# Performance work log

Hardware: AMD Instinct MI355X
Metric: run time of the kernel (lower is better)

## Reference

```python
import jax, jax.numpy as jnp
import numpy as np

V = 100000   # vocab size
H = 1280     # GRU hidden / pic_emb_size
E = 300      # word_emb_size
L = 32       # max_length


def setup_inputs() -> dict:
    key = jax.random.key(0)
    ks = jax.random.split(key, 7)
    s = 0.02  # weight init scale
    return {
        "hidden0": jax.random.normal(ks[0], (H,), jnp.float32),
        "start_emb": jax.random.normal(ks[1], (E,), jnp.float32),
        "W_ih": jax.random.normal(ks[2], (3 * H, E), jnp.float32) * s,
        "W_hh": jax.random.normal(ks[3], (3 * H, H), jnp.float32) * s,
        "b_ih": jnp.zeros((3 * H,), jnp.float32),
        "b_hh": jnp.zeros((3 * H,), jnp.float32),
        "W_cls": jax.random.normal(ks[4], (V, H), jnp.float32) * s,
        "b_cls": jnp.zeros((V,), jnp.float32),
        "vocab_vectors": jax.random.normal(ks[5], (V, E), jnp.float32),
        "max_length": L,
    }


def reference(hidden0, start_emb, W_ih, W_hh, b_ih, b_hh, W_cls, b_cls,
              vocab_vectors, max_length):
    """Autoregressive GRU decode: GRU step -> 1280x100k classifier GEMV ->
    argmax -> embedding gather, for max_length steps (batch=1).
    EOS (token 0) emulated with a `done` mask instead of a Python break.
    Returns (tokens [L] int32, hiddens [L, H] float32)."""

    def step(carry, _):
        h, emb, done = carry
        # PyTorch GRU gate layout: [reset | update | new]
        gi = W_ih @ emb + b_ih               # [3H]
        gh = W_hh @ h + b_hh                 # [3H]
        r = jax.nn.sigmoid(gi[:H] + gh[:H])
        z = jax.nn.sigmoid(gi[H:2 * H] + gh[H:2 * H])
        n = jnp.tanh(gi[2 * H:] + r * gh[2 * H:])
        h_new = jnp.where(done, h, (1.0 - z) * n + z * h)
        logits = W_cls @ h_new + b_cls       # [V] classifier GEMV
        pred = jnp.argmax(logits).astype(jnp.int32)
        token = jnp.where(done, 0, pred)
        done_new = done | (pred == 0)
        emb_new = jnp.where(done_new, emb, vocab_vectors[pred])  # gather next word emb
        return (h_new, emb_new, done_new), (token, h_new)

    init = (hidden0, start_emb, jnp.array(False))
    _, (tokens, hiddens) = jax.lax.scan(step, init, None, length=max_length)
    return tokens, hiddens
```

## Files before the change

kernel.cpp:

```cpp
#include <hip/hip_runtime.h>
#include <math.h>
#include <limits.h>

#define V 100000
#define H 1280
#define E 300
#define L 32
#define G3 (3*H)
#define NBLK 6250

#define WS_H      0
#define WS_EMB    1280
#define WS_GI     1600
#define WS_GH     (WS_GI + G3)
#define WS_SUMABS 9280
#define WS_DONE   9281
#define WS_LOGITS 9284
#define WS_SROW   (WS_LOGITS + V)
#define WS_PLO    (WS_SROW + V)
#define WS_PHI    (WS_PLO + NBLK)
#define WS_Q_BYTEOFF ((size_t)(WS_PHI + NBLK) * 4)
#define WS_BYTES_NEEDED (WS_Q_BYTEOFF + (size_t)V * H)
#define CAND_CAP  256

#define NPART     6250
#define WS_PVAL   WS_LOGITS
#define WS_PIDX   (WS_LOGITS + NPART)

__global__ __launch_bounds__(256)
void init_state(const float* __restrict__ hidden0, const float* __restrict__ start_emb,
                float* __restrict__ ws) {
    int i = blockIdx.x * blockDim.x + threadIdx.x;
    if (i < H) ws[WS_H + i] = hidden0[i];
    if (i < E) ws[WS_EMB + i] = start_emb[i];
    if (i == 0) ((int*)ws)[WS_DONE] = 0;
}

__global__ __launch_bounds__(256)
void convert_int8(const float* __restrict__ W, uint* __restrict__ q_out,
                  float* __restrict__ ws) {
    const int wave = threadIdx.x >> 6;
    const int lane = threadIdx.x & 63;
    const int row = blockIdx.x * 4 + wave;
    const float4* __restrict__ wr = (const float4*)(W + (size_t)row * H);

    float4 v[5];
    float mx = 0.f;
    #pragma unroll
    for (int k = 0; k < 5; ++k) {
        v[k] = wr[lane + 64*k];
        mx = fmaxf(mx, fmaxf(fmaxf(fabsf(v[k].x), fabsf(v[k].y)),
                             fmaxf(fabsf(v[k].z), fabsf(v[k].w))));
    }
    #pragma unroll
    for (int off = 32; off; off >>= 1) mx = fmaxf(mx, __shfl_xor(mx, off));

    float inv = (mx > 0.f) ? 127.0f / mx : 0.f;
    float s   = (mx > 0.f) ? mx / 127.0f : 0.f;

    uint* __restrict__ qrow = q_out + (size_t)row * (H/4);
    #pragma unroll
    for (int k = 0; k < 5; ++k) {
        int q0 = max(-127, min(127, __float2int_rn(v[k].x * inv)));
        int q1 = max(-127, min(127, __float2int_rn(v[k].y * inv)));
        int q2 = max(-127, min(127, __float2int_rn(v[k].z * inv)));
        int q3 = max(-127, min(127, __float2int_rn(v[k].w * inv)));
        qrow[lane + 64*k] = (uint)(q0 & 0xff) | ((uint)(q1 & 0xff) << 8) |
                            ((uint)(q2 & 0xff) << 16) | ((uint)(q3 & 0xff) << 24);
    }
    if (lane == 0) ws[WS_SROW + row] = s;
}

__global__ __launch_bounds__(256)
void gru_matvec(const float* __restrict__ W_ih, const float* __restrict__ W_hh,
                const float* __restrict__ b_ih, const float* __restrict__ b_hh,
                float* __restrict__ ws) {
    if (blockIdx.x == 0 && threadIdx.x == 0) ws[WS_SUMABS] = 0.f;

    const int wave = threadIdx.x >> 6;
    const int lane = threadIdx.x & 63;
    const int row = blockIdx.x * 4 + wave;

    const float4* __restrict__ emb4 = (const float4*)(ws + WS_EMB);
    const float4* __restrict__ h4   = (const float4*)(ws + WS_H);

    const float4* __restrict__ wi = (const float4*)(W_ih + (size_t)row * E);
    float s1 = 0.f;
    for (int i = lane; i < 75; i += 64) {
        float4 w = wi[i], e = emb4[i];
        s1 += w.x*e.x + w.y*e.y + w.z*e.z + w.w*e.w;
    }
    const float4* __restrict__ wh = (const float4*)(W_hh + (size_t)row * H);
    float s2 = 0.f;
    #pragma unroll
    for (int k = 0; k < 5; ++k) {
        float4 w = wh[lane + 64*k], hv = h4[lane + 64*k];
        s2 += w.x*hv.x + w.y*hv.y + w.z*hv.z + w.w*hv.w;
    }
    #pragma unroll
    for (int off = 32; off; off >>= 1) {
        s1 += __shfl_down(s1, off);
        s2 += __shfl_down(s2, off);
    }
    if (lane == 0) {
        ws[WS_GI + row] = s1 + b_ih[row];
        ws[WS_GH + row] = s2 + b_hh[row];
    }
}

__global__ __launch_bounds__(256)
void gru_combine(float* __restrict__ ws, float* __restrict__ hid_out) {
    __shared__ float red[256];
    int tid = threadIdx.x;
    int j = blockIdx.x * 256 + tid;
    int done = ((const int*)ws)[WS_DONE];
    float gir = ws[WS_GI + j], giz = ws[WS_GI + H + j], gin = ws[WS_GI + 2*H + j];
    float ghr = ws[WS_GH + j], ghz = ws[WS_GH + H + j], ghn = ws[WS_GH + 2*H + j];
    float r = 1.f / (1.f + expf(-(gir + ghr)));
    float z = 1.f / (1.f + expf(-(giz + ghz)));
    float n = tanhf(gin + r * ghn);
    float hold = ws[WS_H + j];
    float hnew = done ? hold : (1.f - z) * n + z * hold;
    ws[WS_H + j] = hnew;
    hid_out[j] = hnew;
    red[tid] = fabsf(hnew);
    __syncthreads();
    for (int s = 128; s; s >>= 1) {
        if (tid < s) red[tid] += red[tid + s];
        __syncthreads();
    }
    if (tid == 0) atomicAdd(ws + WS_SUMABS, red[0]);
}

__global__ __launch_bounds__(256)
void cls_int8(const uint* __restrict__ Q, const float* __restrict__ b_cls,
              float* __restrict__ ws) {
    const int wave = threadIdx.x >> 6;
    const int lane = threadIdx.x & 63;
    const int row0 = blockIdx.x * 16 + wave * 4;
    const float4* __restrict__ h4 = (const float4*)(ws + WS_H);

    float4 hv[5];
    #pragma unroll
    for (int k = 0; k < 5; ++k) hv[k] = h4[lane + 64*k];

    const float sumabs = ws[WS_SUMABS];
    float wlo = -INFINITY, whi = -INFINITY;

    for (int rr = 0; rr < 4; ++rr) {
        const int row = row0 + rr;
        const uint* __restrict__ qr = Q + (size_t)row * (H/4);
        float acc = 0.f;
        #pragma unroll
        for (int k = 0; k < 5; ++k) {
            uint u = qr[lane + 64*k];
            float f0 = (float)((int)(u << 24) >> 24);
            float f1 = (float)((int)(u << 16) >> 24);
            float f2 = (float)((int)(u <<  8) >> 24);
            float f3 = (float)((int) u        >> 24);
            acc += f0*hv[k].x + f1*hv[k].y + f2*hv[k].z + f3*hv[k].w;
        }
        #pragma unroll
        for (int off = 32; off; off >>= 1) acc += __shfl_down(acc, off);
        if (lane == 0) {
            float s = ws[WS_SROW + row];
            float q = s * acc + b_cls[row];
            ws[WS_LOGITS + row] = q;
            float e = 0.501f * s * sumabs + 0.002f;
            wlo = fmaxf(wlo, q - e);
            whi = fmaxf(whi, q + e);
        }
    }
    __shared__ float slo[4], shi[4];
    if (lane == 0) { slo[wave] = wlo; shi[wave] = whi; }
    __syncthreads();
    if (threadIdx.x == 0) {
        ws[WS_PLO + blockIdx.x] = fmaxf(fmaxf(slo[0], slo[1]), fmaxf(slo[2], slo[3]));
        ws[WS_PHI + blockIdx.x] = fmaxf(fmaxf(shi[0], shi[1]), fmaxf(shi[2], shi[3]));
    }
}

__global__ __launch_bounds__(1024)
void screen_finalize(float* __restrict__ ws, const float* __restrict__ W_cls,
                     const float* __restrict__ b_cls, const float* __restrict__ vocab,
                     float* __restrict__ tok_out, int t) {
    __shared__ float red[1024];
    __shared__ int   cnt;
    __shared__ int   cidx[CAND_CAP];
    __shared__ float cval[CAND_CAP];
    __shared__ int   s_pred, s_done_new;
    const int tid = threadIdx.x;

    float m = -INFINITY;
    for (int b = tid; b < NBLK; b += 1024) m = fmaxf(m, ws[WS_PLO + b]);
    red[tid] = m;
    __syncthreads();
    for (int s = 512; s; s >>= 1) {
        if (tid < s) red[tid] = fmaxf(red[tid], red[tid + s]);
        __syncthreads();
    }
    m = red[0];
    if (tid == 0) cnt = 0;
    __syncthreads();

    const float sumabs = ws[WS_SUMABS];
    for (int b = tid; b < NBLK; b += 1024) {
        if (ws[WS_PHI + b] >= m) {
            for (int r = b * 16; r < b * 16 + 16; ++r) {
                float s = ws[WS_SROW + r];
                float e = 0.501f * s * sumabs + 0.002f;
                if (ws[WS_LOGITS + r] + e >= m) {
                    int p = atomicAdd(&cnt, 1);
                    if (p < CAND_CAP) cidx[p] = r;
                }
            }
        }
    }
    __syncthreads();
    const int nc = min(cnt, CAND_CAP);

    const int wave = tid >> 6;
    const int lane = tid & 63;
    const float4* __restrict__ h4 = (const float4*)(ws + WS_H);
    for (int c = wave; c < nc; c += 16) {
        int row = cidx[c];
        const float4* __restrict__ wr = (const float4*)(W_cls + (size_t)row * H);
        float s = 0.f;
        #pragma unroll
        for (int k = 0; k < 5; ++k) {
            float4 wv = wr[lane + 64*k], hvv = h4[lane + 64*k];
            s += wv.x*hvv.x + wv.y*hvv.y + wv.z*hvv.z + wv.w*hvv.w;
        }
        #pragma unroll
        for (int off = 32; off; off >>= 1) s += __shfl_down(s, off);
        if (lane == 0) cval[c] = s + b_cls[row];
    }
    __syncthreads();

    if (tid == 0) {
        float bv = -INFINITY; int bi = INT_MAX;
        for (int c = 0; c < nc; ++c) {
            float v = cval[c]; int i = cidx[c];
            if (v > bv || (v == bv && i < bi)) { bv = v; bi = i; }
        }
        int done = ((const int*)ws)[WS_DONE];
        int pred = bi;
        tok_out[t] = (float)(done ? 0 : pred);
        int dn = done | (pred == 0);
        ((int*)ws)[WS_DONE] = dn;
        s_pred = pred; s_done_new = dn;
    }
    __syncthreads();
    if (!s_done_new && tid < E)
        ws[WS_EMB + tid] = vocab[(size_t)s_pred * E + tid];
}

__global__ __launch_bounds__(256)
void logits_argmax_partial(const float* __restrict__ W_cls,
                           const float* __restrict__ b_cls,
                           float* __restrict__ ws) {
    const int wave = threadIdx.x >> 6;
    const int lane = threadIdx.x & 63;
    const int row0 = blockIdx.x * 16 + wave * 4;
    const float4* __restrict__ h4 = (const float4*)(ws + WS_H);

    float best = -INFINITY;
    int bidx = INT_MAX;
    for (int rr = 0; rr < 4; ++rr) {
        const int row = row0 + rr;
        const float4* __restrict__ wr = (const float4*)(W_cls + (size_t)row * H);
        float s = 0.f;
        #pragma unroll
        for (int k = 0; k < 5; ++k) {
            float4 w = wr[lane + 64*k], hv = h4[lane + 64*k];
            s += w.x*hv.x + w.y*hv.y + w.z*hv.z + w.w*hv.w;
        }
        #pragma unroll
        for (int off = 32; off; off >>= 1) s += __shfl_down(s, off);
        if (lane == 0) {
            float logit = s + b_cls[row];
            if (logit > best) { best = logit; bidx = row; }
        }
    }
    __shared__ float sval[4];
    __shared__ int   sidx[4];
    if (lane == 0) { sval[wave] = best; sidx[wave] = bidx; }
    __syncthreads();
    if (threadIdx.x == 0) {
        float bv = sval[0]; int bi = sidx[0];
        #pragma unroll
        for (int w = 1; w < 4; ++w) {
            if (sval[w] > bv || (sval[w] == bv && sidx[w] < bi)) { bv = sval[w]; bi = sidx[w]; }
        }
        ws[WS_PVAL + blockIdx.x] = bv;
        ((int*)ws)[WS_PIDX + blockIdx.x] = bi;
    }
}

__global__ __launch_bounds__(1024)
void argmax_update(float* __restrict__ ws, const float* __restrict__ vocab,
                   float* __restrict__ tok_out, int t) {
    __shared__ float sval[1024];
    __shared__ int   sidx[1024];
    const int tid = threadIdx.x;
    float best = -INFINITY;
    int bidx = INT_MAX;
    for (int i = tid; i < NPART; i += 1024) {
        float v = ws[WS_PVAL + i];
        int  id = ((const int*)ws)[WS_PIDX + i];
        if (v > best || (v == best && id < bidx)) { best = v; bidx = id; }
    }
    sval[tid] = best; sidx[tid] = bidx;
    __syncthreads();
    #pragma unroll
    for (int s = 512; s; s >>= 1) {
        if (tid < s) {
            if (sval[tid+s] > sval[tid] ||
                (sval[tid+s] == sval[tid] && sidx[tid+s] < sidx[tid])) {
                sval[tid] = sval[tid+s]; sidx[tid] = sidx[tid+s];
            }
        }
        __syncthreads();
    }
    __shared__ int s_pred, s_donenew;
    if (tid == 0) {
        int pred = sidx[0];
        int done = ((const int*)ws)[WS_DONE];
        tok_out[t] = (float)(done ? 0 : pred);
        int done_new = done | (pred == 0);
        ((int*)ws)[WS_DONE] = done_new;
        s_pred = pred; s_donenew = done_new;
    }
    __syncthreads();
    if (!s_donenew && tid < E) {
        ws[WS_EMB + tid] = vocab[(size_t)s_pred * E + tid];
    }
}

extern "C" void kernel_launch(void* const* d_in, const int* in_sizes, int n_in,
                              void* d_out, int out_size, void* d_ws, size_t ws_size,
                              hipStream_t stream) {
    const float* hidden0   = (const float*)d_in[0];
    const float* start_emb = (const float*)d_in[1];
    const float* W_ih      = (const float*)d_in[2];
    const float* W_hh      = (const float*)d_in[3];
    const float* b_ih      = (const float*)d_in[4];
    const float* b_hh      = (const float*)d_in[5];
    const float* W_cls     = (const float*)d_in[6];
    const float* b_cls     = (const float*)d_in[7];
    const float* vocab     = (const float*)d_in[8];
    float* out = (float*)d_out;
    float* ws  = (float*)d_ws;

    hipLaunchKernelGGL(init_state, dim3(5), dim3(256), 0, stream, hidden0, start_emb, ws);

    if (ws_size >= WS_BYTES_NEEDED) {
        uint* Q = (uint*)((char*)d_ws + WS_Q_BYTEOFF);
        hipLaunchKernelGGL(convert_int8, dim3(V/4), dim3(256), 0, stream, W_cls, Q, ws);
        for (int t = 0; t < L; ++t) {
            hipLaunchKernelGGL(gru_matvec, dim3(G3/4), dim3(256), 0, stream,
                               W_ih, W_hh, b_ih, b_hh, ws);
            hipLaunchKernelGGL(gru_combine, dim3(5), dim3(256), 0, stream,
                               ws, out + L + (size_t)t * H);
            hipLaunchKernelGGL(cls_int8, dim3(NBLK), dim3(256), 0, stream,
                               Q, b_cls, ws);
            hipLaunchKernelGGL(screen_finalize, dim3(1), dim3(1024), 0, stream,
                               ws, W_cls, b_cls, vocab, out, t);
        }
    } else {
        for (int t = 0; t < L; ++t) {
            hipLaunchKernelGGL(gru_matvec, dim3(G3/4), dim3(256), 0, stream,
                               W_ih, W_hh, b_ih, b_hh, ws);
            hipLaunchKernelGGL(gru_combine, dim3(5), dim3(256), 0, stream,
                               ws, out + L + (size_t)t * H);
            hipLaunchKernelGGL(logits_argmax_partial, dim3(NPART), dim3(256), 0, stream,
                               W_cls, b_cls, ws);
            hipLaunchKernelGGL(argmax_update, dim3(1), dim3(1024), 0, stream,
                               ws, vocab, out, t);
        }
    }
}
```

Measured before the change: 1.860 ms.

## Fuse GRU matvec and gate combine, enlarge classifier blocks, double-buffer hidden

Merges the GRU matvec and gate-combine kernels into one kernel, with one block per hidden unit computing the three gate rows and applying the nonlinearity. This removes a launch and the global round-trip for the gate vectors on each step. The hidden state is ping-ponged between two buffers so the fused kernel can read the old state while writing the new one. The |h| sum is spread over 8 padded atomic slots, and the int8 classifier now does 64 rows per block, which changes the screening granularity used by finalize. Finalize first gathers the passing blocks and then scans their rows in parallel.

```diff
diff --git a/kernel.cpp b/kernel.cpp
--- a/kernel.cpp
+++ b/kernel.cpp
@@ -6,33 +6,35 @@
 #define H 1280
 #define E 300
 #define L 32
-#define G3 (3*H)
-#define NBLK 6250
-
-#define WS_H      0
-#define WS_EMB    1280
-#define WS_GI     1600
-#define WS_GH     (WS_GI + G3)
-#define WS_SUMABS 9280
-#define WS_DONE   9281
-#define WS_LOGITS 9284
+#define NBLK 1563
+
+#define WS_H0     0
+#define WS_H1     1280
+#define WS_EMB    2560
+#define WS_SUM8   2880
+#define WS_DONE   3008
+#define WS_LOGITS 3012
 #define WS_SROW   (WS_LOGITS + V)
 #define WS_PLO    (WS_SROW + V)
 #define WS_PHI    (WS_PLO + NBLK)
-#define WS_Q_BYTEOFF ((size_t)(WS_PHI + NBLK) * 4)
+#define WS_Q_BYTEOFF 824576
 #define WS_BYTES_NEEDED (WS_Q_BYTEOFF + (size_t)V * H)
 #define CAND_CAP  256
-
-#define NPART     6250
-#define WS_PVAL   WS_LOGITS
-#define WS_PIDX   (WS_LOGITS + NPART)
+#define PBLK_CAP  128
+
+#define FB_GI     4000
+#define FB_GH     (FB_GI + 3840)
+#define FB_NPART  6250
+#define FB_PVAL   12000
+#define FB_PIDX   (FB_PVAL + FB_NPART)
 
 __global__ __launch_bounds__(256)
 void init_state(const float* __restrict__ hidden0, const float* __restrict__ start_emb,
                 float* __restrict__ ws) {
     int i = blockIdx.x * blockDim.x + threadIdx.x;
-    if (i < H) ws[WS_H + i] = hidden0[i];
+    if (i < H) ws[WS_H0 + i] = hidden0[i];
     if (i < E) ws[WS_EMB + i] = start_emb[i];
+    if (i < 8) ws[WS_SUM8 + i * 16] = 0.f;
     if (i == 0) ((int*)ws)[WS_DONE] = 0;
 }
 
@@ -71,84 +73,77 @@
     if (lane == 0) ws[WS_SROW + row] = s;
 }
 
-__global__ __launch_bounds__(256)
-void gru_matvec(const float* __restrict__ W_ih, const float* __restrict__ W_hh,
-                const float* __restrict__ b_ih, const float* __restrict__ b_hh,
-                float* __restrict__ ws) {
-    if (blockIdx.x == 0 && threadIdx.x == 0) ws[WS_SUMABS] = 0.f;
-
+__global__ __launch_bounds__(192)
+void gru_fused(const float* __restrict__ W_ih, const float* __restrict__ W_hh,
+               const float* __restrict__ b_ih, const float* __restrict__ b_hh,
+               float* __restrict__ ws, const float* __restrict__ hin,
+               float* __restrict__ hout, float* __restrict__ hid_out) {
+    const int g = threadIdx.x >> 6;
+    const int lane = threadIdx.x & 63;
+    const int j = blockIdx.x;
+    const int row = g * H + j;
+
+    const float4* __restrict__ emb4 = (const float4*)(ws + WS_EMB);
+    const float4* __restrict__ h4   = (const float4*)hin;
+
+    const float4* __restrict__ wi = (const float4*)(W_ih + (size_t)row * E);
+    float si = 0.f;
+    for (int i = lane; i < 75; i += 64) {
+        float4 w = wi[i], e = emb4[i];
+        si += w.x*e.x + w.y*e.y + w.z*e.z + w.w*e.w;
+    }
+    const float4* __restrict__ wh = (const float4*)(W_hh + (size_t)row * H);
+    float sh = 0.f;
+    #pragma unroll
+    for (int k = 0; k < 5; ++k) {
+        float4 w = wh[lane + 64*k], hv = h4[lane + 64*k];
+        sh += w.x*hv.x + w.y*hv.y + w.z*hv.z + w.w*hv.w;
+    }
+    #pragma unroll
+    for (int off = 32; off; off >>= 1) {
+        si += __shfl_down(si, off);
+        sh += __shfl_down(sh, off);
+    }
+    __shared__ float gi_s[3], gh_s[3];
+    if (lane == 0) {
+        gi_s[g] = si + b_ih[row];
+        gh_s[g] = sh + b_hh[row];
+    }
+    __syncthreads();
+    if (threadIdx.x == 0) {
+        float r = 1.f / (1.f + expf(-(gi_s[0] + gh_s[0])));
+        float z = 1.f / (1.f + expf(-(gi_s[1] + gh_s[1])));
+        float n = tanhf(gi_s[2] + r * gh_s[2]);
+        int done = ((const int*)ws)[WS_DONE];
+        float hold = hin[j];
+        float hnew = done ? hold : (1.f - z) * n + z * hold;
+        hout[j] = hnew;
+        hid_out[j] = hnew;
+        atomicAdd(ws + WS_SUM8 + (j & 7) * 16, fabsf(hnew));
+    }
+}
+
+__global__ __launch_bounds__(256)
+void cls_int8(const uint* __restrict__ Q, const float* __restrict__ b_cls,
+              float* __restrict__ ws, const float* __restrict__ h) {
     const int wave = threadIdx.x >> 6;
     const int lane = threadIdx.x & 63;
-    const int row = blockIdx.x * 4 + wave;
-
-    const float4* __restrict__ emb4 = (const float4*)(ws + WS_EMB);
-    const float4* __restrict__ h4   = (const float4*)(ws + WS_H);
-
-    const float4* __restrict__ wi = (const float4*)(W_ih + (size_t)row * E);
-    float s1 = 0.f;
-    for (int i = lane; i < 75; i += 64) {
-        float4 w = wi[i], e = emb4[i];
-        s1 += w.x*e.x + w.y*e.y + w.z*e.z + w.w*e.w;
-    }
-    const float4* __restrict__ wh = (const float4*)(W_hh + (size_t)row * H);
-    float s2 = 0.f;
-    #pragma unroll
-    for (int k = 0; k < 5; ++k) {
-        float4 w = wh[lane + 64*k], hv = h4[lane + 64*k];
-        s2 += w.x*hv.x + w.y*hv.y + w.z*hv.z + w.w*hv.w;
-    }
-    #pragma unroll
-    for (int off = 32; off; off >>= 1) {
-        s1 += __shfl_down(s1, off);
-        s2 += __shfl_down(s2, off);
-    }
-    if (lane == 0) {
-        ws[WS_GI + row] = s1 + b_ih[row];
-        ws[WS_GH + row] = s2 + b_hh[row];
-    }
-}
-
-__global__ __launch_bounds__(256)
-void gru_combine(float* __restrict__ ws, float* __restrict__ hid_out) {
-    __shared__ float red[256];
-    int tid = threadIdx.x;
-    int j = blockIdx.x * 256 + tid;
-    int done = ((const int*)ws)[WS_DONE];
-    float gir = ws[WS_GI + j], giz = ws[WS_GI + H + j], gin = ws[WS_GI + 2*H + j];
-    float ghr = ws[WS_GH + j], ghz = ws[WS_GH + H + j], ghn = ws[WS_GH + 2*H + j];
-    float r = 1.f / (1.f + expf(-(gir + ghr)));
-    float z = 1.f / (1.f + expf(-(giz + ghz)));
-    float n = tanhf(gin + r * ghn);
-    float hold = ws[WS_H + j];
-    float hnew = done ? hold : (1.f - z) * n + z * hold;
-    ws[WS_H + j] = hnew;
-    hid_out[j] = hnew;
-    red[tid] = fabsf(hnew);
-    __syncthreads();
-    for (int s = 128; s; s >>= 1) {
-        if (tid < s) red[tid] += red[tid + s];
-        __syncthreads();
-    }
-    if (tid == 0) atomicAdd(ws + WS_SUMABS, red[0]);
-}
-
-__global__ __launch_bounds__(256)
-void cls_int8(const uint* __restrict__ Q, const float* __restrict__ b_cls,
-              float* __restrict__ ws) {
-    const int wave = threadIdx.x >> 6;
-    const int lane = threadIdx.x & 63;
-    const int row0 = blockIdx.x * 16 + wave * 4;
-    const float4* __restrict__ h4 = (const float4*)(ws + WS_H);
+    const int row0 = blockIdx.x * 64 + wave * 16;
+    const float4* __restrict__ h4 = (const float4*)h;
 
     float4 hv[5];
     #pragma unroll
     for (int k = 0; k < 5; ++k) hv[k] = h4[lane + 64*k];
 
-    const float sumabs = ws[WS_SUMABS];
+    float sumabs = 0.f;
+    #pragma unroll
+    for (int i = 0; i < 8; ++i) sumabs += ws[WS_SUM8 + i * 16];
+
     float wlo = -INFINITY, whi = -INFINITY;
 
-    for (int rr = 0; rr < 4; ++rr) {
+    for (int rr = 0; rr < 16; ++rr) {
         const int row = row0 + rr;
+        if (row >= V) break;
         const uint* __restrict__ qr = Q + (size_t)row * (H/4);
         float acc = 0.f;
         #pragma unroll
@@ -181,16 +176,21 @@
 }
 
 __global__ __launch_bounds__(1024)
-void screen_finalize(float* __restrict__ ws, const float* __restrict__ W_cls,
-                     const float* __restrict__ b_cls, const float* __restrict__ vocab,
-                     float* __restrict__ tok_out, int t) {
+void finalize(float* __restrict__ ws, const float* __restrict__ W_cls,
+              const float* __restrict__ b_cls, const float* __restrict__ vocab,
+              float* __restrict__ tok_out, int t, const float* __restrict__ h) {
     __shared__ float red[1024];
-    __shared__ int   cnt;
+    __shared__ int   npass, cnt;
+    __shared__ int   pblk[PBLK_CAP];
     __shared__ int   cidx[CAND_CAP];
     __shared__ float cval[CAND_CAP];
     __shared__ int   s_pred, s_done_new;
     const int tid = threadIdx.x;
 
+    float sumabs = 0.f;
+    #pragma unroll
+    for (int i = 0; i < 8; ++i) sumabs += ws[WS_SUM8 + i * 16];
+
     float m = -INFINITY;
     for (int b = tid; b < NBLK; b += 1024) m = fmaxf(m, ws[WS_PLO + b]);
     red[tid] = m;
@@ -200,19 +200,26 @@
         __syncthreads();
     }
     m = red[0];
-    if (tid == 0) cnt = 0;
-    __syncthreads();
-
-    const float sumabs = ws[WS_SUMABS];
+    if (tid == 0) { npass = 0; cnt = 0; }
+    __syncthreads();
+
     for (int b = tid; b < NBLK; b += 1024) {
         if (ws[WS_PHI + b] >= m) {
-            for (int r = b * 16; r < b * 16 + 16; ++r) {
-                float s = ws[WS_SROW + r];
-                float e = 0.501f * s * sumabs + 0.002f;
-                if (ws[WS_LOGITS + r] + e >= m) {
-                    int p = atomicAdd(&cnt, 1);
-                    if (p < CAND_CAP) cidx[p] = r;
-                }
+            int p = atomicAdd(&npass, 1);
+            if (p < PBLK_CAP) pblk[p] = b;
+        }
+    }
+    __syncthreads();
+    const int np = min(npass, PBLK_CAP);
+
+    for (int k = tid; k < np * 64; k += 1024) {
+        int row = pblk[k >> 6] * 64 + (k & 63);
+        if (row < V) {
+            float s = ws[WS_SROW + row];
+            float e = 0.501f * s * sumabs + 0.002f;
+            if (ws[WS_LOGITS + row] + e >= m) {
+                int p = atomicAdd(&cnt, 1);
+                if (p < CAND_CAP) cidx[p] = row;
             }
         }
     }
@@ -221,7 +228,7 @@
 
     const int wave = tid >> 6;
     const int lane = tid & 63;
-    const float4* __restrict__ h4 = (const float4*)(ws + WS_H);
+    const float4* __restrict__ h4 = (const float4*)h;
     for (int c = wave; c < nc; c += 16) {
         int row = cidx[c];
         const float4* __restrict__ wr = (const float4*)(W_cls + (size_t)row * H);
@@ -253,17 +260,65 @@
     __syncthreads();
     if (!s_done_new && tid < E)
         ws[WS_EMB + tid] = vocab[(size_t)s_pred * E + tid];
-}
-
-__global__ __launch_bounds__(256)
-void logits_argmax_partial(const float* __restrict__ W_cls,
-                           const float* __restrict__ b_cls,
-                           float* __restrict__ ws) {
+    if (tid < 8) ws[WS_SUM8 + tid * 16] = 0.f;
+}
+
+__global__ __launch_bounds__(256)
+void fb_gru_matvec(const float* __restrict__ W_ih, const float* __restrict__ W_hh,
+                   const float* __restrict__ b_ih, const float* __restrict__ b_hh,
+                   float* __restrict__ ws) {
+    const int wave = threadIdx.x >> 6;
+    const int lane = threadIdx.x & 63;
+    const int row = blockIdx.x * 4 + wave;
+    const float4* __restrict__ emb4 = (const float4*)(ws + WS_EMB);
+    const float4* __restrict__ h4   = (const float4*)(ws + WS_H0);
+    const float4* __restrict__ wi = (const float4*)(W_ih + (size_t)row * E);
+    float s1 = 0.f;
+    for (int i = lane; i < 75; i += 64) {
+        float4 w = wi[i], e = emb4[i];
+        s1 += w.x*e.x + w.y*e.y + w.z*e.z + w.w*e.w;
+    }
+    const float4* __restrict__ wh = (const float4*)(W_hh + (size_t)row * H);
+    float s2 = 0.f;
+    #pragma unroll
+    for (int k = 0; k < 5; ++k) {
+        float4 w = wh[lane + 64*k], hv = h4[lane + 64*k];
+        s2 += w.x*hv.x + w.y*hv.y + w.z*hv.z + w.w*hv.w;
+    }
+    #pragma unroll
+    for (int off = 32; off; off >>= 1) {
+        s1 += __shfl_down(s1, off);
+        s2 += __shfl_down(s2, off);
+    }
+    if (lane == 0) {
+        ws[FB_GI + row] = s1 + b_ih[row];
+        ws[FB_GH + row] = s2 + b_hh[row];
+    }
+}
+
+__global__ __launch_bounds__(256)
+void fb_gru_combine(float* __restrict__ ws, float* __restrict__ hid_out) {
+    int j = blockIdx.x * 256 + threadIdx.x;
+    if (j >= H) return;
+    int done = ((const int*)ws)[WS_DONE];
+    float gir = ws[FB_GI + j], giz = ws[FB_GI + H + j], gin = ws[FB_GI + 2*H + j];
+    float ghr = ws[FB_GH + j], ghz = ws[FB_GH + H + j], ghn = ws[FB_GH + 2*H + j];
+    float r = 1.f / (1.f + expf(-(gir + ghr)));
+    float z = 1.f / (1.f + expf(-(giz + ghz)));
+    float n = tanhf(gin + r * ghn);
+    float hold = ws[WS_H0 + j];
+    float hnew = done ? hold : (1.f - z) * n + z * hold;
+    ws[WS_H0 + j] = hnew;
+    hid_out[j] = hnew;
+}
+
+__global__ __launch_bounds__(256)
+void fb_logits_argmax(const float* __restrict__ W_cls, const float* __restrict__ b_cls,
+                      float* __restrict__ ws) {
     const int wave = threadIdx.x >> 6;
     const int lane = threadIdx.x & 63;
     const int row0 = blockIdx.x * 16 + wave * 4;
-    const float4* __restrict__ h4 = (const float4*)(ws + WS_H);
-
+    const float4* __restrict__ h4 = (const float4*)(ws + WS_H0);
     float best = -INFINITY;
     int bidx = INT_MAX;
     for (int rr = 0; rr < 4; ++rr) {
@@ -289,25 +344,24 @@
     if (threadIdx.x == 0) {
         float bv = sval[0]; int bi = sidx[0];
         #pragma unroll
-        for (int w = 1; w < 4; ++w) {
+        for (int w = 1; w < 4; ++w)
             if (sval[w] > bv || (sval[w] == bv && sidx[w] < bi)) { bv = sval[w]; bi = sidx[w]; }
-        }
-        ws[WS_PVAL + blockIdx.x] = bv;
-        ((int*)ws)[WS_PIDX + blockIdx.x] = bi;
+        ws[FB_PVAL + blockIdx.x] = bv;
+        ((int*)ws)[FB_PIDX + blockIdx.x] = bi;
     }
 }
 
 __global__ __launch_bounds__(1024)
-void argmax_update(float* __restrict__ ws, const float* __restrict__ vocab,
-                   float* __restrict__ tok_out, int t) {
+void fb_argmax_update(float* __restrict__ ws, const float* __restrict__ vocab,
+                      float* __restrict__ tok_out, int t) {
     __shared__ float sval[1024];
     __shared__ int   sidx[1024];
     const int tid = threadIdx.x;
     float best = -INFINITY;
     int bidx = INT_MAX;
-    for (int i = tid; i < NPART; i += 1024) {
-        float v = ws[WS_PVAL + i];
-        int  id = ((const int*)ws)[WS_PIDX + i];
+    for (int i = tid; i < FB_NPART; i += 1024) {
+        float v = ws[FB_PVAL + i];
+        int  id = ((const int*)ws)[FB_PIDX + i];
         if (v > best || (v == best && id < bidx)) { best = v; bidx = id; }
     }
     sval[tid] = best; sidx[tid] = bidx;
@@ -332,9 +386,8 @@
         s_pred = pred; s_donenew = done_new;
     }
     __syncthreads();
-    if (!s_donenew && tid < E) {
+    if (!s_donenew && tid < E)
         ws[WS_EMB + tid] = vocab[(size_t)s_pred * E + tid];
-    }
 }
 
 extern "C" void kernel_launch(void* const* d_in, const int* in_sizes, int n_in,
@@ -358,24 +411,25 @@
         uint* Q = (uint*)((char*)d_ws + WS_Q_BYTEOFF);
         hipLaunchKernelGGL(convert_int8, dim3(V/4), dim3(256), 0, stream, W_cls, Q, ws);
         for (int t = 0; t < L; ++t) {
-            hipLaunchKernelGGL(gru_matvec, dim3(G3/4), dim3(256), 0, stream,
-                               W_ih, W_hh, b_ih, b_hh, ws);
-            hipLaunchKernelGGL(gru_combine, dim3(5), dim3(256), 0, stream,
-                               ws, out + L + (size_t)t * H);
+            const float* hin = ws + ((t & 1) ? WS_H1 : WS_H0);
+            float* hout      = ws + ((t & 1) ? WS_H0 : WS_H1);
+            hipLaunchKernelGGL(gru_fused, dim3(H), dim3(192), 0, stream,
+                               W_ih, W_hh, b_ih, b_hh, ws, hin, hout,
+                               out + L + (size_t)t * H);
             hipLaunchKernelGGL(cls_int8, dim3(NBLK), dim3(256), 0, stream,
-                               Q, b_cls, ws);
-            hipLaunchKernelGGL(screen_finalize, dim3(1), dim3(1024), 0, stream,
-                               ws, W_cls, b_cls, vocab, out, t);
+                               Q, b_cls, ws, hout);
+            hipLaunchKernelGGL(finalize, dim3(1), dim3(1024), 0, stream,
+                               ws, W_cls, b_cls, vocab, out, t, hout);
         }
     } else {
         for (int t = 0; t < L; ++t) {
-            hipLaunchKernelGGL(gru_matvec, dim3(G3/4), dim3(256), 0, stream,
+            hipLaunchKernelGGL(fb_gru_matvec, dim3(960), dim3(256), 0, stream,
                                W_ih, W_hh, b_ih, b_hh, ws);
-            hipLaunchKernelGGL(gru_combine, dim3(5), dim3(256), 0, stream,
+            hipLaunchKernelGGL(fb_gru_combine, dim3(5), dim3(256), 0, stream,
                                ws, out + L + (size_t)t * H);
-            hipLaunchKernelGGL(logits_argmax_partial, dim3(NPART), dim3(256), 0, stream,
+            hipLaunchKernelGGL(fb_logits_argmax, dim3(FB_NPART), dim3(256), 0, stream,
                                W_cls, b_cls, ws);
-            hipLaunchKernelGGL(argmax_update, dim3(1), dim3(1024), 0, stream,
+            hipLaunchKernelGGL(fb_argmax_update, dim3(1), dim3(1024), 0, stream,
                                ws, vocab, out, t);
         }
     }
```

New measurement: 1.539 ms. 17.2% less time.
